# Performance work log

Hardware: AMD Instinct MI355X
Metric: run time of the kernel (lower is better)

## Reference

```python
import jax, jax.numpy as jnp
import numpy as np
from jax import lax

EPS = 1e-08


def setup_inputs() -> dict:
    key = jax.random.key(0)
    k1, k2, k3 = jax.random.split(key, 3)
    B, I, O, H, W_, K = 16, 512, 512, 32, 32, 3
    x = jax.random.normal(k1, (B, I, H, W_), dtype=jnp.float32)
    s = jax.random.uniform(k2, (B, I), dtype=jnp.float32)
    weight = jax.random.normal(k3, (O, I, K, K), dtype=jnp.float32)
    return {"x": x, "s": s, "weight": weight}


def reference(x, s, weight):
    # x: [B, I, H, W], s: [B, I], weight: [O, I, kH, kW]
    B, I, H, Wd = x.shape
    O = weight.shape[0]
    # Per-sample modulated weights: [B, O, I, kH, kW]
    # (faithful to source: the weight_scale multiply is dead code, overwritten)
    Wm = s[:, None, :, None, None] * weight[None]
    # Demodulation: L2-normalize each per-sample output filter
    sigma = jnp.sqrt(jnp.sum(Wm * Wm, axis=(2, 3, 4), keepdims=True) + EPS)
    Wm = Wm / sigma
    # Grouped conv with groups = batch_size (same trick as torch source)
    x_g = x.reshape(1, B * I, H, Wd)
    W_g = Wm.reshape(B * O, I, *weight.shape[-2:])
    out = lax.conv_general_dilated(
        x_g, W_g,
        window_strides=(1, 1),
        padding='SAME',
        feature_group_count=B,
        dimension_numbers=('NCHW', 'OIHW', 'NCHW'),
    )
    return out.reshape(B, O, out.shape[-2], out.shape[-1])
```

## Files before the change

kernel.cpp:

```cpp
#include <hip/hip_runtime.h>
#include <hip/hip_bf16.h>
#include <stdint.h>

#define BATCH 16
#define CIN   512
#define COUT  512
#define HH    32
#define WW    32
#define HP    34
#define HWN   1024
#define EPS_  1e-8f

#define NTILES 72
#define SLOTA  16384
#define SLOTB  32768
#define LDS_BYTES (3*(SLOTA+SLOTB))

typedef __attribute__((ext_vector_type(8))) short bf16x8;
typedef __attribute__((ext_vector_type(4))) float f32x4;
typedef __attribute__((address_space(1))) void gvoid;
typedef __attribute__((address_space(3))) void lvoid;

#define XS_OFF    0
#define XS_BYTES  (BATCH*HP*HP*CIN*2)
#define WT_OFF    (XS_OFF + XS_BYTES)
#define WT_BYTES  (9*COUT*CIN*2)
#define ISG_OFF   (WT_OFF + WT_BYTES)

__global__ __launch_bounds__(256)
void wprep(const float* __restrict__ w, const float* __restrict__ s,
           __hip_bfloat16* __restrict__ wt, float* __restrict__ isg) {
  __shared__ float s2[BATCH * CIN];
  __shared__ float red[16][4];
  const int o = blockIdx.x;
  const int t = threadIdx.x;

  for (int j = t; j < BATCH * CIN; j += 256) {
    float v = s[j];
    s2[j] = v * v;
  }

  float ss[2];
#pragma unroll
  for (int u = 0; u < 2; ++u) {
    int i = t + u * 256;
    const float* wp = w + ((size_t)o * CIN + i) * 9;
    float acc = 0.f;
#pragma unroll
    for (int k = 0; k < 9; ++k) {
      float v = wp[k];
      acc += v * v;
      __hip_bfloat16 hb = __float2bfloat16(v);
      wt[(size_t)k * COUT * CIN + o * CIN + i] = hb;
    }
    ss[u] = acc;
  }
  __syncthreads();

  float accb[16];
#pragma unroll
  for (int b = 0; b < 16; ++b) accb[b] = 0.f;
#pragma unroll
  for (int u = 0; u < 2; ++u) {
    int i = t + u * 256;
    float q = ss[u];
#pragma unroll
    for (int b = 0; b < 16; ++b) accb[b] += q * s2[b * CIN + i];
  }
#pragma unroll
  for (int b = 0; b < 16; ++b) {
#pragma unroll
    for (int off = 32; off; off >>= 1) accb[b] += __shfl_xor(accb[b], off);
    if ((t & 63) == 0) red[b][t >> 6] = accb[b];
  }
  __syncthreads();
  if (t < 16) {
    float tot = red[t][0] + red[t][1] + red[t][2] + red[t][3];
    isg[t * COUT + o] = 1.0f / sqrtf(tot + EPS_);
  }
}

__global__ __launch_bounds__(256)
void pack3(const float* __restrict__ x, const float* __restrict__ s,
           __hip_bfloat16* __restrict__ xs) {
  const int bid = blockIdx.x;
  const int hp = bid % 34;
  const int b = bid / 34;
  const int tid = threadIdx.x;
  __hip_bfloat16* rowbase = xs + (((size_t)(b * HP + hp)) * HP) * CIN;

  if (hp == 0 || hp == 33) {
    for (int j = tid; j < HP * CIN / 8; j += 256)
      ((int4*)rowbase)[j] = make_int4(0, 0, 0, 0);
    return;
  }
  if (tid < 64)        ((int4*)rowbase)[tid] = make_int4(0, 0, 0, 0);
  else if (tid < 128)  ((int4*)(rowbase + 33 * CIN))[tid - 64] = make_int4(0, 0, 0, 0);

  __shared__ unsigned short tile[32][520];
  __shared__ float ssh[CIN];
  ssh[tid]       = s[b * CIN + tid];
  ssh[256 + tid] = s[b * CIN + 256 + tid];
  __syncthreads();

  const int h = hp - 1;
  const int r = tid >> 3;
  const int c = tid & 7;
  const float* xbase = x + (size_t)b * CIN * HWN + h * WW;
#pragma unroll
  for (int p = 0; p < 16; ++p) {
    int i = p * 32 + r;
    float4 v = *(const float4*)(xbase + (size_t)i * HWN + c * 4);
    float sc = ssh[i];
#pragma unroll
    for (int j = 0; j < 4; ++j) {
      float f = ((const float*)&v)[j] * sc;
      __hip_bfloat16 hb = __float2bfloat16(f);
      tile[c * 4 + j][i] = *(unsigned short*)&hb;
    }
  }
  __syncthreads();

  const int wq = tid >> 3;
  const int i0 = (tid & 7) * 64;
  __hip_bfloat16* dst = rowbase + (wq + 1) * CIN + i0;
  const int4* src = (const int4*)&tile[wq][i0];
#pragma unroll
  for (int q = 0; q < 8; ++q)
    ((int4*)dst)[q] = src[q];
}

__global__ __launch_bounds__(512, 2)
void conv_mfma8(const __hip_bfloat16* __restrict__ xs,
                const __hip_bfloat16* __restrict__ wt,
                const float* __restrict__ isg,
                float* __restrict__ out) {
  extern __shared__ __align__(16) char lds[];
  char* ldsA = lds;
  char* ldsB = lds + 3 * SLOTA;

  const int bid = blockIdx.x;
  const int lin = (bid & 7) * 32 + (bid >> 3);
  const int b  = lin >> 4;
  const int mt = (lin >> 2) & 3;
  const int nt = lin & 3;
  const int m0  = mt * 128;
  const int hw0 = nt * 256;

  const int t  = threadIdx.x;
  const int wv = t >> 6;
  const int l  = t & 63;
  const int wr = wv >> 2;
  const int wc = wv & 3;

  int baseA[2], baseB[4];
  const int swz = (l & 7) ^ (l >> 3);
#pragma unroll
  for (int q = 0; q < 2; ++q) {
    int r = (wv * 2 + q) * 8 + (l >> 3);
    baseA[q] = (m0 + r) * CIN + swz * 8;
  }
#pragma unroll
  for (int q = 0; q < 4; ++q) {
    int r = (wv * 4 + q) * 8 + (l >> 3);
    int n_abs = hw0 + r;
    int hB = n_abs >> 5, wB = n_abs & 31;
    baseB[q] = ((b * HP + hB) * HP + wB) * CIN + swz * 8;
  }

  int offA[2][4], offB[2][4];
#pragma unroll
  for (int kk = 0; kk < 2; ++kk) {
#pragma unroll
    for (int f = 0; f < 4; ++f) {
      int slot16 = ((kk * 4) + (l >> 4)) ^ (l & 7);
      offA[kk][f] = (wr * 64 + f * 16 + (l & 15)) * 128 + slot16 * 16;
      offB[kk][f] = (wc * 64 + f * 16 + (l & 15)) * 128 + slot16 * 16;
    }
  }

  f32x4 acc[4][4];
#pragma unroll
  for (int m = 0; m < 4; ++m)
#pragma unroll
    for (int n = 0; n < 4; ++n)
      acc[m][n] = (f32x4){0.f, 0.f, 0.f, 0.f};

#define TILE_OFFS(tt, gA, gB)                                   \
  {                                                             \
    int tap = (tt) >> 3, ic = (tt) & 7;                         \
    int kh = (tap * 11) >> 5;                                   \
    int kw = tap - kh * 3;                                      \
    gA = tap * (COUT * CIN) + ic * 64;                          \
    gB = (kh * HP + kw) * CIN + ic * 64;                        \
  }

#define STAGE_A(q, gA, sl)                                                  \
  __builtin_amdgcn_global_load_lds(                                         \
      (gvoid*)(const void*)(wt + (gA) + baseA[q]),                          \
      (lvoid*)(ldsA + (sl) * SLOTA + (wv * 2 + (q)) * 1024), 16, 0, 0)
#define STAGE_B(q, gB, sl)                                                  \
  __builtin_amdgcn_global_load_lds(                                         \
      (gvoid*)(const void*)(xs + (gB) + baseB[q]),                          \
      (lvoid*)(ldsB + (sl) * SLOTB + (wv * 4 + (q)) * 1024), 16, 0, 0)

  {
    int gA, gB;
    TILE_OFFS(0, gA, gB);
    STAGE_A(0, gA, 0); STAGE_A(1, gA, 0);
    STAGE_B(0, gB, 0); STAGE_B(1, gB, 0); STAGE_B(2, gB, 0); STAGE_B(3, gB, 0);
    TILE_OFFS(1, gA, gB);
    STAGE_A(0, gA, 1); STAGE_A(1, gA, 1);
    STAGE_B(0, gB, 1); STAGE_B(1, gB, 1); STAGE_B(2, gB, 1); STAGE_B(3, gB, 1);
  }
  asm volatile("s_waitcnt vmcnt(6)" ::: "memory");
  __builtin_amdgcn_s_barrier();

#define PHASE(mp, kk, STAGES)                                                         \
  {                                                                                   \
    bf16x8 af0 = *(const bf16x8*)(pA + offA[kk][2 * (mp)]);                           \
    bf16x8 af1 = *(const bf16x8*)(pA + offA[kk][2 * (mp) + 1]);                       \
    if ((mp) == 0) {                                                                  \
      bfr0 = *(const bf16x8*)(pB + offB[kk][0]);                                      \
      bfr1 = *(const bf16x8*)(pB + offB[kk][1]);                                      \
      bfr2 = *(const bf16x8*)(pB + offB[kk][2]);                                      \
      bfr3 = *(const bf16x8*)(pB + offB[kk][3]);                                      \
    }                                                                                 \
    STAGES;                                                                           \
    __builtin_amdgcn_s_barrier();                                                     \
    __builtin_amdgcn_s_setprio(1);                                                    \
    acc[2*(mp)][0]   = __builtin_amdgcn_mfma_f32_16x16x32_bf16(af0, bfr0, acc[2*(mp)][0],   0,0,0); \
    acc[2*(mp)][1]   = __builtin_amdgcn_mfma_f32_16x16x32_bf16(af0, bfr1, acc[2*(mp)][1],   0,0,0); \
    acc[2*(mp)][2]   = __builtin_amdgcn_mfma_f32_16x16x32_bf16(af0, bfr2, acc[2*(mp)][2],   0,0,0); \
    acc[2*(mp)][3]   = __builtin_amdgcn_mfma_f32_16x16x32_bf16(af0, bfr3, acc[2*(mp)][3],   0,0,0); \
    acc[2*(mp)+1][0] = __builtin_amdgcn_mfma_f32_16x16x32_bf16(af1, bfr0, acc[2*(mp)+1][0], 0,0,0); \
    acc[2*(mp)+1][1] = __builtin_amdgcn_mfma_f32_16x16x32_bf16(af1, bfr1, acc[2*(mp)+1][1], 0,0,0); \
    acc[2*(mp)+1][2] = __builtin_amdgcn_mfma_f32_16x16x32_bf16(af1, bfr2, acc[2*(mp)+1][2], 0,0,0); \
    acc[2*(mp)+1][3] = __builtin_amdgcn_mfma_f32_16x16x32_bf16(af1, bfr3, acc[2*(mp)+1][3], 0,0,0); \
    __builtin_amdgcn_s_setprio(0);                                                    \
    __builtin_amdgcn_s_barrier();                                                     \
  }

  int cur = 0, s2 = 2;
  bf16x8 bfr0, bfr1, bfr2, bfr3;
  for (int tt = 0; tt < NTILES; ++tt) {
    int t2 = tt + 2;
    if (t2 >= NTILES) t2 = NTILES - 1;
    int gA2, gB2;
    TILE_OFFS(t2, gA2, gB2);
    const char* pA = ldsA + cur * SLOTA;
    const char* pB = ldsB + cur * SLOTB;

    PHASE(0, 0, { STAGE_A(0, gA2, s2); STAGE_A(1, gA2, s2); });
    PHASE(1, 0, { STAGE_B(0, gB2, s2); STAGE_B(1, gB2, s2); });
    PHASE(0, 1, { STAGE_B(2, gB2, s2); });
    PHASE(1, 1, { STAGE_B(3, gB2, s2);
                  asm volatile("s_waitcnt vmcnt(6)" ::: "memory"); });

    cur = (cur == 2) ? 0 : cur + 1;
    s2  = (s2  == 2) ? 0 : s2  + 1;
  }

#pragma unroll
  for (int m = 0; m < 4; ++m) {
#pragma unroll
    for (int j = 0; j < 4; ++j) {
      int o = m0 + wr * 64 + m * 16 + (l >> 4) * 4 + j;
      float sg = isg[b * COUT + o];
      float* orow = out + ((size_t)(b * COUT + o)) * HWN + hw0 + wc * 64 + (l & 15);
#pragma unroll
      for (int n = 0; n < 4; ++n)
        orow[n * 16] = acc[m][n][j] * sg;
    }
  }
}

extern "C" void kernel_launch(void* const* d_in, const int* in_sizes, int n_in,
                              void* d_out, int out_size, void* d_ws, size_t ws_size,
                              hipStream_t stream) {
  const float* x = (const float*)d_in[0];
  const float* s = (const float*)d_in[1];
  const float* w = (const float*)d_in[2];
  float* out = (float*)d_out;
  char* ws = (char*)d_ws;
  __hip_bfloat16* xs  = (__hip_bfloat16*)(ws + XS_OFF);
  __hip_bfloat16* wt  = (__hip_bfloat16*)(ws + WT_OFF);
  float*          isg = (float*)(ws + ISG_OFF);

  (void)hipFuncSetAttribute((const void*)conv_mfma8,
                            hipFuncAttributeMaxDynamicSharedMemorySize, LDS_BYTES);

  hipLaunchKernelGGL(wprep, dim3(COUT), dim3(256), 0, stream, w, s, wt, isg);
  hipLaunchKernelGGL(pack3, dim3(BATCH * 34), dim3(256), 0, stream, x, s, xs);
  hipLaunchKernelGGL(conv_mfma8, dim3(256), dim3(512), LDS_BYTES, stream,
                     xs, wt, isg, out);
}
```

Baseline: 170.2 us.

## Load weight fragments directly to registers and merge prep kernels into one launch

The conv kernel no longer stages the weight (A) tile through LDS. Each wave loads its A fragments straight from global memory into registers one tile ahead, double-buffered in registers, while only the activation (B) tile stays in a 3-slot LDS ring. Each tile now has one barrier instead of eight, which cuts LDS traffic and synchronisation but raises register pressure and exposes global-load latency on A. The two prep kernels are also fused into a single launch to save one kernel launch gap.

```diff
diff --git a/kernel.cpp b/kernel.cpp
--- a/kernel.cpp
+++ b/kernel.cpp
@@ -12,9 +12,8 @@
 #define EPS_  1e-8f
 
 #define NTILES 72
-#define SLOTA  16384
 #define SLOTB  32768
-#define LDS_BYTES (3*(SLOTA+SLOTB))
+#define LDS_BYTES (3*SLOTB)
 
 typedef __attribute__((ext_vector_type(8))) short bf16x8;
 typedef __attribute__((ext_vector_type(4))) float f32x4;
@@ -28,116 +27,111 @@
 #define ISG_OFF   (WT_OFF + WT_BYTES)
 
 __global__ __launch_bounds__(256)
-void wprep(const float* __restrict__ w, const float* __restrict__ s,
-           __hip_bfloat16* __restrict__ wt, float* __restrict__ isg) {
-  __shared__ float s2[BATCH * CIN];
-  __shared__ float red[16][4];
-  const int o = blockIdx.x;
-  const int t = threadIdx.x;
-
-  for (int j = t; j < BATCH * CIN; j += 256) {
-    float v = s[j];
-    s2[j] = v * v;
-  }
-
-  float ss[2];
-#pragma unroll
-  for (int u = 0; u < 2; ++u) {
-    int i = t + u * 256;
-    const float* wp = w + ((size_t)o * CIN + i) * 9;
-    float acc = 0.f;
-#pragma unroll
-    for (int k = 0; k < 9; ++k) {
-      float v = wp[k];
-      acc += v * v;
-      __hip_bfloat16 hb = __float2bfloat16(v);
-      wt[(size_t)k * COUT * CIN + o * CIN + i] = hb;
-    }
-    ss[u] = acc;
-  }
-  __syncthreads();
-
-  float accb[16];
-#pragma unroll
-  for (int b = 0; b < 16; ++b) accb[b] = 0.f;
-#pragma unroll
-  for (int u = 0; u < 2; ++u) {
-    int i = t + u * 256;
-    float q = ss[u];
-#pragma unroll
-    for (int b = 0; b < 16; ++b) accb[b] += q * s2[b * CIN + i];
-  }
-#pragma unroll
-  for (int b = 0; b < 16; ++b) {
-#pragma unroll
-    for (int off = 32; off; off >>= 1) accb[b] += __shfl_xor(accb[b], off);
-    if ((t & 63) == 0) red[b][t >> 6] = accb[b];
-  }
-  __syncthreads();
-  if (t < 16) {
-    float tot = red[t][0] + red[t][1] + red[t][2] + red[t][3];
-    isg[t * COUT + o] = 1.0f / sqrtf(tot + EPS_);
+void prep_all(const float* __restrict__ x, const float* __restrict__ s,
+              const float* __restrict__ w,
+              __hip_bfloat16* __restrict__ xs, __hip_bfloat16* __restrict__ wt,
+              float* __restrict__ isg) {
+  __shared__ __align__(16) char smem[35328];
+  const int bid = blockIdx.x;
+  const int tid = threadIdx.x;
+
+  if (bid < BATCH * 34) {
+    unsigned short (*tile)[520] = (unsigned short (*)[520])smem;
+    float* ssh = (float*)(smem + 33280);
+    const int hp = bid % 34;
+    const int b  = bid / 34;
+    __hip_bfloat16* rowbase = xs + (((size_t)(b * HP + hp)) * HP) * CIN;
+
+    if (hp == 0 || hp == 33) {
+      for (int j = tid; j < HP * CIN / 8; j += 256)
+        ((int4*)rowbase)[j] = make_int4(0, 0, 0, 0);
+      return;
+    }
+    if (tid < 64)        ((int4*)rowbase)[tid] = make_int4(0, 0, 0, 0);
+    else if (tid < 128)  ((int4*)(rowbase + 33 * CIN))[tid - 64] = make_int4(0, 0, 0, 0);
+
+    ssh[tid]       = s[b * CIN + tid];
+    ssh[256 + tid] = s[b * CIN + 256 + tid];
+    __syncthreads();
+
+    const int h = hp - 1;
+    const int r = tid >> 3;
+    const int c = tid & 7;
+    const float* xbase = x + (size_t)b * CIN * HWN + h * WW;
+#pragma unroll
+    for (int p = 0; p < 16; ++p) {
+      int i = p * 32 + r;
+      float4 v = *(const float4*)(xbase + (size_t)i * HWN + c * 4);
+      float sc = ssh[i];
+#pragma unroll
+      for (int j = 0; j < 4; ++j) {
+        float f = ((const float*)&v)[j] * sc;
+        __hip_bfloat16 hb = __float2bfloat16(f);
+        tile[c * 4 + j][i] = *(unsigned short*)&hb;
+      }
+    }
+    __syncthreads();
+
+    const int wq = tid >> 3;
+    const int i0 = (tid & 7) * 64;
+    __hip_bfloat16* dst = rowbase + (wq + 1) * CIN + i0;
+    const int4* src = (const int4*)&tile[wq][i0];
+#pragma unroll
+    for (int q = 0; q < 8; ++q)
+      ((int4*)dst)[q] = src[q];
+  } else {
+    float* s2  = (float*)smem;
+    float (*red)[4] = (float (*)[4])(smem + 32768);
+    const int o = bid - BATCH * 34;
+    for (int j = tid; j < BATCH * CIN; j += 256) {
+      float v = s[j];
+      s2[j] = v * v;
+    }
+    float ss[2];
+#pragma unroll
+    for (int u = 0; u < 2; ++u) {
+      int i = tid + u * 256;
+      const float* wp = w + ((size_t)o * CIN + i) * 9;
+      float acc = 0.f;
+#pragma unroll
+      for (int k = 0; k < 9; ++k) {
+        float v = wp[k];
+        acc += v * v;
+        wt[(size_t)k * COUT * CIN + o * CIN + i] = __float2bfloat16(v);
+      }
+      ss[u] = acc;
+    }
+    __syncthreads();
+    float accb[16];
+#pragma unroll
+    for (int b = 0; b < 16; ++b) accb[b] = 0.f;
+#pragma unroll
+    for (int u = 0; u < 2; ++u) {
+      int i = tid + u * 256;
+      float q = ss[u];
+#pragma unroll
+      for (int b = 0; b < 16; ++b) accb[b] += q * s2[b * CIN + i];
+    }
+#pragma unroll
+    for (int b = 0; b < 16; ++b) {
+#pragma unroll
+      for (int off = 32; off; off >>= 1) accb[b] += __shfl_xor(accb[b], off);
+      if ((tid & 63) == 0) red[b][tid >> 6] = accb[b];
+    }
+    __syncthreads();
+    if (tid < 16) {
+      float tot = red[tid][0] + red[tid][1] + red[tid][2] + red[tid][3];
+      isg[tid * COUT + o] = 1.0f / sqrtf(tot + EPS_);
+    }
   }
 }
 
-__global__ __launch_bounds__(256)
-void pack3(const float* __restrict__ x, const float* __restrict__ s,
-           __hip_bfloat16* __restrict__ xs) {
-  const int bid = blockIdx.x;
-  const int hp = bid % 34;
-  const int b = bid / 34;
-  const int tid = threadIdx.x;
-  __hip_bfloat16* rowbase = xs + (((size_t)(b * HP + hp)) * HP) * CIN;
-
-  if (hp == 0 || hp == 33) {
-    for (int j = tid; j < HP * CIN / 8; j += 256)
-      ((int4*)rowbase)[j] = make_int4(0, 0, 0, 0);
-    return;
-  }
-  if (tid < 64)        ((int4*)rowbase)[tid] = make_int4(0, 0, 0, 0);
-  else if (tid < 128)  ((int4*)(rowbase + 33 * CIN))[tid - 64] = make_int4(0, 0, 0, 0);
-
-  __shared__ unsigned short tile[32][520];
-  __shared__ float ssh[CIN];
-  ssh[tid]       = s[b * CIN + tid];
-  ssh[256 + tid] = s[b * CIN + 256 + tid];
-  __syncthreads();
-
-  const int h = hp - 1;
-  const int r = tid >> 3;
-  const int c = tid & 7;
-  const float* xbase = x + (size_t)b * CIN * HWN + h * WW;
-#pragma unroll
-  for (int p = 0; p < 16; ++p) {
-    int i = p * 32 + r;
-    float4 v = *(const float4*)(xbase + (size_t)i * HWN + c * 4);
-    float sc = ssh[i];
-#pragma unroll
-    for (int j = 0; j < 4; ++j) {
-      float f = ((const float*)&v)[j] * sc;
-      __hip_bfloat16 hb = __float2bfloat16(f);
-      tile[c * 4 + j][i] = *(unsigned short*)&hb;
-    }
-  }
-  __syncthreads();
-
-  const int wq = tid >> 3;
-  const int i0 = (tid & 7) * 64;
-  __hip_bfloat16* dst = rowbase + (wq + 1) * CIN + i0;
-  const int4* src = (const int4*)&tile[wq][i0];
-#pragma unroll
-  for (int q = 0; q < 8; ++q)
-    ((int4*)dst)[q] = src[q];
-}
-
 __global__ __launch_bounds__(512, 2)
-void conv_mfma8(const __hip_bfloat16* __restrict__ xs,
-                const __hip_bfloat16* __restrict__ wt,
-                const float* __restrict__ isg,
-                float* __restrict__ out) {
-  extern __shared__ __align__(16) char lds[];
-  char* ldsA = lds;
-  char* ldsB = lds + 3 * SLOTA;
+void conv_v3(const __hip_bfloat16* __restrict__ xs,
+             const __hip_bfloat16* __restrict__ wt,
+             const float* __restrict__ isg,
+             float* __restrict__ out) {
+  extern __shared__ __align__(16) char ldsB[];
 
   const int bid = blockIdx.x;
   const int lin = (bid & 7) * 32 + (bid >> 3);
@@ -153,13 +147,8 @@
   const int wr = wv >> 2;
   const int wc = wv & 3;
 
-  int baseA[2], baseB[4];
+  int baseB[4];
   const int swz = (l & 7) ^ (l >> 3);
-#pragma unroll
-  for (int q = 0; q < 2; ++q) {
-    int r = (wv * 2 + q) * 8 + (l >> 3);
-    baseA[q] = (m0 + r) * CIN + swz * 8;
-  }
 #pragma unroll
   for (int q = 0; q < 4; ++q) {
     int r = (wv * 4 + q) * 8 + (l >> 3);
@@ -168,16 +157,21 @@
     baseB[q] = ((b * HP + hB) * HP + wB) * CIN + swz * 8;
   }
 
-  int offA[2][4], offB[2][4];
-#pragma unroll
-  for (int kk = 0; kk < 2; ++kk) {
+  int offB[2][4];
+#pragma unroll
+  for (int kk = 0; kk < 2; ++kk)
 #pragma unroll
     for (int f = 0; f < 4; ++f) {
       int slot16 = ((kk * 4) + (l >> 4)) ^ (l & 7);
-      offA[kk][f] = (wr * 64 + f * 16 + (l & 15)) * 128 + slot16 * 16;
       offB[kk][f] = (wc * 64 + f * 16 + (l & 15)) * 128 + slot16 * 16;
     }
-  }
+
+  int ark[2][4];
+#pragma unroll
+  for (int kk = 0; kk < 2; ++kk)
+#pragma unroll
+    for (int mf = 0; mf < 4; ++mf)
+      ark[kk][mf] = (m0 + wr * 64 + mf * 16 + (l & 15)) * CIN + kk * 32 + (l >> 4) * 8;
 
   f32x4 acc[4][4];
 #pragma unroll
@@ -186,80 +180,96 @@
     for (int n = 0; n < 4; ++n)
       acc[m][n] = (f32x4){0.f, 0.f, 0.f, 0.f};
 
-#define TILE_OFFS(tt, gA, gB)                                   \
-  {                                                             \
-    int tap = (tt) >> 3, ic = (tt) & 7;                         \
-    int kh = (tap * 11) >> 5;                                   \
-    int kw = tap - kh * 3;                                      \
-    gA = tap * (COUT * CIN) + ic * 64;                          \
-    gB = (kh * HP + kw) * CIN + ic * 64;                        \
-  }
-
-#define STAGE_A(q, gA, sl)                                                  \
-  __builtin_amdgcn_global_load_lds(                                         \
-      (gvoid*)(const void*)(wt + (gA) + baseA[q]),                          \
-      (lvoid*)(ldsA + (sl) * SLOTA + (wv * 2 + (q)) * 1024), 16, 0, 0)
+#define MF(a, bb, c) __builtin_amdgcn_mfma_f32_16x16x32_bf16(a, bb, c, 0, 0, 0)
+
 #define STAGE_B(q, gB, sl)                                                  \
   __builtin_amdgcn_global_load_lds(                                         \
       (gvoid*)(const void*)(xs + (gB) + baseB[q]),                          \
       (lvoid*)(ldsB + (sl) * SLOTB + (wv * 4 + (q)) * 1024), 16, 0, 0)
 
-  {
-    int gA, gB;
-    TILE_OFFS(0, gA, gB);
-    STAGE_A(0, gA, 0); STAGE_A(1, gA, 0);
-    STAGE_B(0, gB, 0); STAGE_B(1, gB, 0); STAGE_B(2, gB, 0); STAGE_B(3, gB, 0);
-    TILE_OFFS(1, gA, gB);
-    STAGE_A(0, gA, 1); STAGE_A(1, gA, 1);
-    STAGE_B(0, gB, 1); STAGE_B(1, gB, 1); STAGE_B(2, gB, 1); STAGE_B(3, gB, 1);
-  }
-  asm volatile("s_waitcnt vmcnt(6)" ::: "memory");
+#define LOAD_A(AN, tti)                                                     \
+  {                                                                         \
+    int tap_ = (tti) >> 3, ic_ = (tti) & 7;                                 \
+    const __hip_bfloat16* ap_ = wt + (size_t)tap_ * (COUT * CIN) + ic_ * 64;\
+    AN[0][0] = *(const bf16x8*)(ap_ + ark[0][0]);                           \
+    AN[0][1] = *(const bf16x8*)(ap_ + ark[0][1]);                           \
+    AN[0][2] = *(const bf16x8*)(ap_ + ark[0][2]);                           \
+    AN[0][3] = *(const bf16x8*)(ap_ + ark[0][3]);                           \
+    AN[1][0] = *(const bf16x8*)(ap_ + ark[1][0]);                           \
+    AN[1][1] = *(const bf16x8*)(ap_ + ark[1][1]);                           \
+    AN[1][2] = *(const bf16x8*)(ap_ + ark[1][2]);                           \
+    AN[1][3] = *(const bf16x8*)(ap_ + ark[1][3]);                           \
+  }
+
+#define STAGE_TILE_B(tti, sl)                                               \
+  {                                                                         \
+    int tap_ = (tti) >> 3, ic_ = (tti) & 7;                                 \
+    int kh_ = tap_ / 3, kw_ = tap_ - kh_ * 3;                               \
+    int gB_ = (kh_ * HP + kw_) * CIN + ic_ * 64;                            \
+    STAGE_B(0, gB_, sl); STAGE_B(1, gB_, sl);                               \
+    STAGE_B(2, gB_, sl); STAGE_B(3, gB_, sl);                               \
+  }
+
+#define KK_PHASE(kk, AC)                                                    \
+  {                                                                         \
+    bf16x8 b0 = *(const bf16x8*)(pB + offB[kk][0]);                         \
+    bf16x8 b1 = *(const bf16x8*)(pB + offB[kk][1]);                         \
+    bf16x8 b2 = *(const bf16x8*)(pB + offB[kk][2]);                         \
+    bf16x8 b3 = *(const bf16x8*)(pB + offB[kk][3]);                         \
+    __builtin_amdgcn_s_setprio(1);                                          \
+    acc[0][0] = MF(AC[kk][0], b0, acc[0][0]);                               \
+    acc[0][1] = MF(AC[kk][0], b1, acc[0][1]);                               \
+    acc[0][2] = MF(AC[kk][0], b2, acc[0][2]);                               \
+    acc[0][3] = MF(AC[kk][0], b3, acc[0][3]);                               \
+    acc[1][0] = MF(AC[kk][1], b0, acc[1][0]);                               \
+    acc[1][1] = MF(AC[kk][1], b1, acc[1][1]);                               \
+    acc[1][2] = MF(AC[kk][1], b2, acc[1][2]);                               \
+    acc[1][3] = MF(AC[kk][1], b3, acc[1][3]);                               \
+    acc[2][0] = MF(AC[kk][2], b0, acc[2][0]);                               \
+    acc[2][1] = MF(AC[kk][2], b1, acc[2][1]);                               \
+    acc[2][2] = MF(AC[kk][2], b2, acc[2][2]);                               \
+    acc[2][3] = MF(AC[kk][2], b3, acc[2][3]);                               \
+    acc[3][0] = MF(AC[kk][3], b0, acc[3][0]);                               \
+    acc[3][1] = MF(AC[kk][3], b1, acc[3][1]);                               \
+    acc[3][2] = MF(AC[kk][3], b2, acc[3][2]);                               \
+    acc[3][3] = MF(AC[kk][3], b3, acc[3][3]);                               \
+    __builtin_amdgcn_s_setprio(0);                                          \
+  }
+
+#define TILE(AC, AN, tt)                                                    \
+  {                                                                         \
+    int t1 = (tt) + 1; if (t1 >= NTILES) t1 = NTILES - 1;                   \
+    int t2 = (tt) + 2; if (t2 >= NTILES) t2 = NTILES - 1;                   \
+    LOAD_A(AN, t1);                                                         \
+    STAGE_TILE_B(t2, sl2);                                                  \
+    const char* pB = ldsB + cur * SLOTB;                                    \
+    KK_PHASE(0, AC);                                                        \
+    KK_PHASE(1, AC);                                                        \
+    asm volatile("s_waitcnt lgkmcnt(0)" ::: "memory");                      \
+    asm volatile("s_waitcnt vmcnt(4)" ::: "memory");                        \
+    __builtin_amdgcn_sched_barrier(0);                                      \
+    __builtin_amdgcn_s_barrier();                                           \
+    __builtin_amdgcn_sched_barrier(0);                                      \
+    cur = (cur == 2) ? 0 : cur + 1;                                         \
+    sl2 = (sl2 == 2) ? 0 : sl2 + 1;                                         \
+  }
+
+  bf16x8 a0[2][4], a1[2][4];
+  STAGE_TILE_B(0, 0);
+  STAGE_TILE_B(1, 1);
+  LOAD_A(a0, 0);
+  asm volatile("s_waitcnt vmcnt(4)" ::: "memory");
+  __builtin_amdgcn_sched_barrier(0);
   __builtin_amdgcn_s_barrier();
-
-#define PHASE(mp, kk, STAGES)                                                         \
-  {                                                                                   \
-    bf16x8 af0 = *(const bf16x8*)(pA + offA[kk][2 * (mp)]);                           \
-    bf16x8 af1 = *(const bf16x8*)(pA + offA[kk][2 * (mp) + 1]);                       \
-    if ((mp) == 0) {                                                                  \
-      bfr0 = *(const bf16x8*)(pB + offB[kk][0]);                                      \
-      bfr1 = *(const bf16x8*)(pB + offB[kk][1]);                                      \
-      bfr2 = *(const bf16x8*)(pB + offB[kk][2]);                                      \
-      bfr3 = *(const bf16x8*)(pB + offB[kk][3]);                                      \
-    }                                                                                 \
-    STAGES;                                                                           \
-    __builtin_amdgcn_s_barrier();                                                     \
-    __builtin_amdgcn_s_setprio(1);                                                    \
-    acc[2*(mp)][0]   = __builtin_amdgcn_mfma_f32_16x16x32_bf16(af0, bfr0, acc[2*(mp)][0],   0,0,0); \
-    acc[2*(mp)][1]   = __builtin_amdgcn_mfma_f32_16x16x32_bf16(af0, bfr1, acc[2*(mp)][1],   0,0,0); \
-    acc[2*(mp)][2]   = __builtin_amdgcn_mfma_f32_16x16x32_bf16(af0, bfr2, acc[2*(mp)][2],   0,0,0); \
-    acc[2*(mp)][3]   = __builtin_amdgcn_mfma_f32_16x16x32_bf16(af0, bfr3, acc[2*(mp)][3],   0,0,0); \
-    acc[2*(mp)+1][0] = __builtin_amdgcn_mfma_f32_16x16x32_bf16(af1, bfr0, acc[2*(mp)+1][0], 0,0,0); \
-    acc[2*(mp)+1][1] = __builtin_amdgcn_mfma_f32_16x16x32_bf16(af1, bfr1, acc[2*(mp)+1][1], 0,0,0); \
-    acc[2*(mp)+1][2] = __builtin_amdgcn_mfma_f32_16x16x32_bf16(af1, bfr2, acc[2*(mp)+1][2], 0,0,0); \
-    acc[2*(mp)+1][3] = __builtin_amdgcn_mfma_f32_16x16x32_bf16(af1, bfr3, acc[2*(mp)+1][3], 0,0,0); \
-    __builtin_amdgcn_s_setprio(0);                                                    \
-    __builtin_amdgcn_s_barrier();                                                     \
-  }
-
-  int cur = 0, s2 = 2;
-  bf16x8 bfr0, bfr1, bfr2, bfr3;
-  for (int tt = 0; tt < NTILES; ++tt) {
-    int t2 = tt + 2;
-    if (t2 >= NTILES) t2 = NTILES - 1;
-    int gA2, gB2;
-    TILE_OFFS(t2, gA2, gB2);
-    const char* pA = ldsA + cur * SLOTA;
-    const char* pB = ldsB + cur * SLOTB;
-
-    PHASE(0, 0, { STAGE_A(0, gA2, s2); STAGE_A(1, gA2, s2); });
-    PHASE(1, 0, { STAGE_B(0, gB2, s2); STAGE_B(1, gB2, s2); });
-    PHASE(0, 1, { STAGE_B(2, gB2, s2); });
-    PHASE(1, 1, { STAGE_B(3, gB2, s2);
-                  asm volatile("s_waitcnt vmcnt(6)" ::: "memory"); });
-
-    cur = (cur == 2) ? 0 : cur + 1;
-    s2  = (s2  == 2) ? 0 : s2  + 1;
-  }
+  __builtin_amdgcn_sched_barrier(0);
+
+  int cur = 0, sl2 = 2;
+#pragma unroll 1
+  for (int tt = 0; tt < NTILES; tt += 2) {
+    TILE(a0, a1, tt);
+    TILE(a1, a0, tt + 1);
+  }
+  asm volatile("s_waitcnt vmcnt(0)" ::: "memory");
 
 #pragma unroll
   for (int m = 0; m < 4; ++m) {
@@ -287,11 +297,11 @@
   __hip_bfloat16* wt  = (__hip_bfloat16*)(ws + WT_OFF);
   float*          isg = (float*)(ws + ISG_OFF);
 
-  (void)hipFuncSetAttribute((const void*)conv_mfma8,
+  (void)hipFuncSetAttribute((const void*)conv_v3,
                             hipFuncAttributeMaxDynamicSharedMemorySize, LDS_BYTES);
 
-  hipLaunchKernelGGL(wprep, dim3(COUT), dim3(256), 0, stream, w, s, wt, isg);
-  hipLaunchKernelGGL(pack3, dim3(BATCH * 34), dim3(256), 0, stream, x, s, xs);
-  hipLaunchKernelGGL(conv_mfma8, dim3(256), dim3(512), LDS_BYTES, stream,
+  hipLaunchKernelGGL(prep_all, dim3(BATCH * 34 + COUT), dim3(256), 0, stream,
+                     x, s, w, xs, wt, isg);
+  hipLaunchKernelGGL(conv_v3, dim3(256), dim3(512), LDS_BYTES, stream,
                      xs, wt, isg, out);
 }
```

New measurement: 276.7 us. 1.63x slower.
